# Optimization experiments

Measured on AMD Instinct MI355X. Metric: run time of the kernel, lower is better.

The kernel has to match this reference:

```python
import jax, jax.numpy as jnp
import numpy as np

K = 512      # fixed candidate budget per pyramid level (batched stand-in for mask.nonzero)
THR = 0.5    # candidate threshold from `p > 0.5`
CUBE = 4     # z-2 : z+2 -> 4-voxel cube per axis


def _conv3d(x, w, b, stride):
    y = jax.lax.conv_general_dilated(
        x, w, (stride, stride, stride), 'SAME',
        dimension_numbers=('NCDHW', 'OIDHW', 'NCDHW'))
    return y + b[None, :, None, None, None]


def _up2(x):
    return jnp.repeat(jnp.repeat(jnp.repeat(x, 2, axis=2), 2, axis=3), 2, axis=4)


def _extract(p):
    # p: [1, C, D, H, W] -> (cubes [K, C, 4, 4, 4], valid [K])
    p0 = p[0]
    C, D, H, W = p0.shape
    score = p0.max(axis=0)                       # [D, H, W] peak over channels
    vals, idx = jax.lax.top_k(score.reshape(-1), K)
    valid = (vals > THR).astype(p0.dtype)        # mask out sub-threshold slots
    z = idx // (H * W)
    rem = idx % (H * W)
    y = rem // W
    x = rem % W
    zs = jnp.clip(z - 2, 0, D - CUBE)
    ys = jnp.clip(y - 2, 0, H - CUBE)
    xs = jnp.clip(x - 2, 0, W - CUBE)

    def cube(zi, yi, xi):
        return jax.lax.dynamic_slice(p0, (0, zi, yi, xi), (C, CUBE, CUBE, CUBE))

    return jax.vmap(cube)(zs, ys, xs), valid


def _lhi(cubes):
    # local intensity descriptor: per-channel mean + std over the cube
    m = cubes.mean(axis=(2, 3, 4))
    s = jnp.sqrt(cubes.var(axis=(2, 3, 4)) + 1e-6)
    return jnp.concatenate([m, s], axis=-1)      # [K, 2C]


def _forward(x, c1w, c1b, c2w, c2b, c3w, c3b,
             l1w, l1b, l2w, l2b, l3w, l3b, w1, b1, w2, b2):
    # Encoder3D: 3 strided conv blocks
    f1 = jax.nn.relu(_conv3d(x, c1w, c1b, 2))    # [1,16,48,96,96]
    f2 = jax.nn.relu(_conv3d(f1, c2w, c2b, 2))   # [1,32,24,48,48]
    f3 = jax.nn.relu(_conv3d(f2, c3w, c3b, 2))   # [1,64,12,24,24]
    # FeaturePyramid3D: laterals + top-down adds
    p3 = _conv3d(f3, l3w, l3b, 1)
    p2 = _conv3d(f2, l2w, l2b, 1) + _up2(p3)
    p1 = _conv3d(f1, l1w, l1b, 1) + _up2(p2)
    outs = []
    for p in (p1, p2, p3):
        cubes, valid = _extract(p)
        lhi = _lhi(cubes)                        # [K, 64]
        h = jax.nn.relu(lhi @ w1 + b1)
        o = (h @ w2 + b2) * valid[:, None]       # zero out invalid candidate slots
        outs.append(o)
    return jnp.concatenate(outs, axis=0)         # [3K, 2]


def setup_inputs() -> dict:
    key = jax.random.key(0)
    ks = jax.random.split(key, 10)

    def w(k, shape, scale):
        return jax.random.normal(k, shape, jnp.float32) * scale

    return {
        'x':   jax.random.normal(ks[0], (1, 1, 96, 192, 192), jnp.float32),
        'c1w': w(ks[1], (16, 1, 3, 3, 3), 0.3),  'c1b': jnp.zeros((16,), jnp.float32),
        'c2w': w(ks[2], (32, 16, 3, 3, 3), 0.1), 'c2b': jnp.zeros((32,), jnp.float32),
        'c3w': w(ks[3], (64, 32, 3, 3, 3), 0.08), 'c3b': jnp.zeros((64,), jnp.float32),
        'l1w': w(ks[4], (32, 16, 1, 1, 1), 0.3), 'l1b': jnp.zeros((32,), jnp.float32),
        'l2w': w(ks[5], (32, 32, 1, 1, 1), 0.3), 'l2b': jnp.zeros((32,), jnp.float32),
        'l3w': w(ks[6], (32, 64, 1, 1, 1), 0.3), 'l3b': jnp.zeros((32,), jnp.float32),
        'w1':  w(ks[7], (64, 128), 0.2),         'b1':  jnp.zeros((128,), jnp.float32),
        'w2':  w(ks[8], (128, 2), 0.2),          'b2':  jnp.zeros((2,), jnp.float32),
    }


def reference(x, c1w, c1b, c2w, c2b, c3w, c3b,
              l1w, l1b, l2w, l2b, l3w, l3b, w1, b1, w2, b2):
    return _forward(x, c1w, c1b, c2w, c2b, c3w, c3b,
                    l1w, l1b, l2w, l2b, l3w, l3b, w1, b1, w2, b2)
```

## Files before the change

kernel.cpp:

```cpp
#include <hip/hip_runtime.h>
#include <hip/hip_bf16.h>
#include <cstdint>
#include <cstddef>

#define N1 442368
#define N2 55296
#define N3 6912

#define PZ1 9409
#define PN1 461041
#define PV1 461041
#define PZ2 2401
#define PN2 60025
#define PV2 60025

#define MAP1(x) (((x) & 1) ? 49 + ((x) >> 1) : ((x) >> 1))
#define MAP2(x) (((x) & 1) ? 25 + ((x) >> 1) : ((x) >> 1))

#define KCAND 512
#define CAP   4096

__device__ __forceinline__ unsigned long long f2key64(double f) {
  unsigned long long b = (unsigned long long)__double_as_longlong(f);
  return (b & 0x8000000000000000ULL) ? ~b : (b | 0x8000000000000000ULL);
}
__device__ __forceinline__ unsigned f2key32(float f) {
  unsigned b = __float_as_uint(f);
  return (b & 0x80000000u) ? ~b : (b | 0x80000000u);
}

__global__ void convert_k(const float* __restrict__ c1w, const float* __restrict__ c2w,
                          const float* __restrict__ c3w, const float* __restrict__ l1w,
                          const float* __restrict__ l2w, const float* __restrict__ l3w,
                          double* __restrict__ wd1, double* __restrict__ wd2,
                          double* __restrict__ wd3, double* __restrict__ wl1,
                          double* __restrict__ wl2, double* __restrict__ wl3) {
  int seg = blockIdx.y;
  int i = blockIdx.x * 256 + threadIdx.x;
  if (seg == 0) {
    if (i < 432) { int c = i & 15, t = i >> 4; wd1[i] = (double)c1w[c * 27 + t]; }
  } else if (seg == 1) {
    if (i < 13824) {
      int c = i & 31, t = (i >> 5) % 27, ci = i / 864;
      wd2[i] = (double)c2w[(c * 16 + ci) * 27 + t];
    }
  } else if (seg == 2) {
    if (i < 55296) {
      int c = i & 3, t = (i >> 2) % 27, ci = (i / 108) & 31, g = i / 3456;
      wd3[i] = (double)c3w[((g * 4 + c) * 32 + ci) * 27 + t];
    }
  } else if (seg == 3) {
    if (i < 512) { int c = i & 31, ci = i >> 5; wl1[i] = (double)l1w[c * 16 + ci]; }
  } else if (seg == 4) {
    if (i < 1024) { int c = i & 31, ci = i >> 5; wl2[i] = (double)l2w[c * 32 + ci]; }
  } else {
    if (i < 2048) { int c = i & 31, ci = i >> 5; wl3[i] = (double)l3w[c * 64 + ci]; }
  }
}

__global__ __launch_bounds__(256) void conv1_k(const float* __restrict__ x, const double* __restrict__ wd1,
                                               const float* __restrict__ b, double* __restrict__ f1) {
  int v = blockIdx.x * 256 + threadIdx.x;
  if (v >= PV1) return;
  int z = v / PZ1; int r = v % PZ1; int y = r / 97; int xo = r % 97;
  int ov = z * PZ1 + y * 97 + MAP1(xo);
  if (z >= 48 || y >= 96 || xo >= 96) {
#pragma unroll
    for (int c = 0; c < 16; c++) f1[(size_t)c * PN1 + ov] = 0.0;
    return;
  }
  float val[27];
#pragma unroll
  for (int dz = 0; dz < 3; dz++)
#pragma unroll
    for (int dy = 0; dy < 3; dy++)
#pragma unroll
      for (int dx = 0; dx < 3; dx++) {
        int zi = 2 * z + dz, yi = 2 * y + dy, xi = 2 * xo + dx;
        bool ok = (zi < 96) & (yi < 192) & (xi < 192);
        int zc = min(zi, 95), yc = min(yi, 191), xc = min(xi, 191);
        float t = x[(zc * 192 + yc) * 192 + xc];
        val[(dz * 3 + dy) * 3 + dx] = ok ? t : 0.0f;
      }
  double acc[16];
#pragma unroll
  for (int c = 0; c < 16; c++) acc[c] = (double)b[c];
#pragma unroll
  for (int t = 0; t < 27; t++) {
    double vv = (double)val[t];
#pragma unroll
    for (int c = 0; c < 16; c++) acc[c] = fma(vv, wd1[t * 16 + c], acc[c]);
  }
#pragma unroll
  for (int c = 0; c < 16; c++) f1[(size_t)c * PN1 + ov] = fmax(acc[c], 0.0);
}

__global__ __launch_bounds__(256, 2) void conv2_k(const double* __restrict__ f1, const double* __restrict__ wd2,
                                                  const float* __restrict__ b, double* __restrict__ f2) {
  int v = blockIdx.x * 256 + threadIdx.x;
  if (v >= PV2) return;
  int z = v / PZ2; int r = v % PZ2; int y = r / 49; int xo = r % 49;
  int ov = z * PZ2 + y * 49 + MAP2(xo);
  if (z >= 24 || y >= 48 || xo >= 48) {
#pragma unroll
    for (int c = 0; c < 32; c++) f2[(size_t)c * PN2 + ov] = 0.0;
    return;
  }
  double acc[32];
#pragma unroll
  for (int c = 0; c < 32; c++) acc[c] = (double)b[c];
  const double* base = f1 + (size_t)(2 * z) * PZ1 + (2 * y) * 97;
  for (int ci = 0; ci < 16; ci++) {
    const double* fp = base + (size_t)ci * PN1;
    double vals[27];
#pragma unroll
    for (int dz = 0; dz < 3; dz++)
#pragma unroll
      for (int dy = 0; dy < 3; dy++) {
        const double* row = fp + dz * PZ1 + dy * 97;
        int o = (dz * 3 + dy) * 3;
        vals[o + 0] = row[xo];
        vals[o + 1] = row[49 + xo];
        vals[o + 2] = row[xo + 1];
      }
#pragma unroll
    for (int t = 0; t < 27; t++) {
      double vv = vals[t];
      const double* w32 = wd2 + (ci * 27 + t) * 32;
#pragma unroll
      for (int c = 0; c < 32; c++) acc[c] = fma(vv, w32[c], acc[c]);
    }
  }
#pragma unroll
  for (int c = 0; c < 32; c++) f2[(size_t)c * PN2 + ov] = fmax(acc[c], 0.0);
}

__global__ __launch_bounds__(256, 2) void conv3_k(const double* __restrict__ f2, const double* __restrict__ wd3,
                                                  const float* __restrict__ b, double* __restrict__ f3) {
  int g = blockIdx.y;
  int v = blockIdx.x * 256 + threadIdx.x;
  if (v >= N3) return;
  int z = v / 576; int r = v % 576; int y = r / 24; int xo = r % 24;
  double acc[4];
#pragma unroll
  for (int c = 0; c < 4; c++) acc[c] = (double)b[g * 4 + c];
  const double* wp = wd3 + (size_t)g * 3456;
  const double* base = f2 + (size_t)(2 * z) * PZ2 + (2 * y) * 49;
  for (int ci = 0; ci < 32; ci++) {
    const double* fp = base + (size_t)ci * PN2;
    double vals[27];
#pragma unroll
    for (int dz = 0; dz < 3; dz++)
#pragma unroll
      for (int dy = 0; dy < 3; dy++) {
        const double* row = fp + dz * PZ2 + dy * 49;
        int o = (dz * 3 + dy) * 3;
        vals[o + 0] = row[xo];
        vals[o + 1] = row[25 + xo];
        vals[o + 2] = row[xo + 1];
      }
#pragma unroll
    for (int t = 0; t < 27; t++) {
      double vv = vals[t];
      const double* w4 = wp + (ci * 27 + t) * 4;
#pragma unroll
      for (int c = 0; c < 4; c++) acc[c] = fma(vv, w4[c], acc[c]);
    }
  }
#pragma unroll
  for (int c = 0; c < 4; c++) f3[(size_t)(g * 4 + c) * N3 + v] = fmax(acc[c], 0.0);
}

__global__ __launch_bounds__(256) void p3_k(const double* __restrict__ f3, const double* __restrict__ wl3,
                                            const float* __restrict__ b, double* __restrict__ p3d,
                                            float* __restrict__ p3f, double* __restrict__ s3,
                                            float* __restrict__ s3f) {
  int v = blockIdx.x * 256 + threadIdx.x;
  if (v >= N3) return;
  double acc[32];
#pragma unroll
  for (int c = 0; c < 32; c++) acc[c] = (double)b[c];
  for (int ci = 0; ci < 64; ci++) {
    double vv = f3[(size_t)ci * N3 + v];
    const double* wp = wl3 + ci * 32;
#pragma unroll
    for (int c = 0; c < 32; c++) acc[c] = fma(vv, wp[c], acc[c]);
  }
  double m = -1e300;
#pragma unroll
  for (int c = 0; c < 32; c++) {
    p3d[(size_t)c * N3 + v] = acc[c];
    p3f[(size_t)c * N3 + v] = (float)acc[c];
    m = fmax(m, acc[c]);
  }
  s3[v] = m;
  s3f[v] = (float)m;
}

__global__ __launch_bounds__(256) void p2_k(const double* __restrict__ f2, const double* __restrict__ wl2,
                                            const float* __restrict__ b, const double* __restrict__ p3d,
                                            double* __restrict__ p2d, float* __restrict__ p2f,
                                            double* __restrict__ s2, float* __restrict__ s2f) {
  int v = blockIdx.x * 256 + threadIdx.x;
  if (v >= N2) return;
  int z = v / (48 * 48); int r = v % (48 * 48); int y = r / 48; int xo = r % 48;
  int pidx = z * PZ2 + y * 49 + MAP2(xo);
  int up = ((z >> 1) * 24 + (y >> 1)) * 24 + (xo >> 1);
  double acc[32];
#pragma unroll
  for (int c = 0; c < 32; c++) acc[c] = (double)b[c];
  for (int ci = 0; ci < 32; ci++) {
    double vv = f2[(size_t)ci * PN2 + pidx];
    const double* wp = wl2 + ci * 32;
#pragma unroll
    for (int c = 0; c < 32; c++) acc[c] = fma(vv, wp[c], acc[c]);
  }
  double m = -1e300;
#pragma unroll
  for (int c = 0; c < 32; c++) {
    double o = acc[c] + p3d[(size_t)c * N3 + up];
    p2d[(size_t)c * N2 + v] = o;
    p2f[(size_t)c * N2 + v] = (float)o;
    m = fmax(m, o);
  }
  s2[v] = m;
  s2f[v] = (float)m;
}

__global__ __launch_bounds__(256) void p1_k(const double* __restrict__ f1, const double* __restrict__ wl1,
                                            const float* __restrict__ b, const double* __restrict__ p2d,
                                            double* __restrict__ s1, float* __restrict__ s1f) {
  int v = blockIdx.x * 256 + threadIdx.x;
  if (v >= N1) return;
  int z = v / (96 * 96); int r = v % (96 * 96); int y = r / 96; int xo = r % 96;
  int pidx = z * PZ1 + y * 97 + MAP1(xo);
  int up = ((z >> 1) * 48 + (y >> 1)) * 48 + (xo >> 1);
  double acc[32];
#pragma unroll
  for (int c = 0; c < 32; c++) acc[c] = (double)b[c];
  for (int ci = 0; ci < 16; ci++) {
    double vv = f1[(size_t)ci * PN1 + pidx];
    const double* wp = wl1 + ci * 32;
#pragma unroll
    for (int c = 0; c < 32; c++) acc[c] = fma(vv, wp[c], acc[c]);
  }
  double m = -1e300;
#pragma unroll
  for (int c = 0; c < 32; c++) m = fmax(m, acc[c] + p2d[(size_t)c * N2 + up]);
  s1[v] = m;
  s1f[v] = (float)m;
}

__global__ void hist1_k(const float* __restrict__ s1, const float* __restrict__ s2,
                        const float* __restrict__ s3, unsigned* __restrict__ hist) {
  int L = blockIdx.y;
  const float* s = L == 0 ? s1 : (L == 1 ? s2 : s3);
  int n = L == 0 ? N1 : (L == 1 ? N2 : N3);
  unsigned* hg = hist + L * 256;
  __shared__ unsigned h[256];
  h[threadIdx.x] = 0;
  __syncthreads();
  for (int i = blockIdx.x * 256 + threadIdx.x; i < n; i += gridDim.x * 256)
    atomicAdd(&h[f2key32(s[i]) >> 24], 1u);
  __syncthreads();
  unsigned v = h[threadIdx.x];
  if (v) atomicAdd(&hg[threadIdx.x], v);
}

__global__ void hist2_k(const float* __restrict__ s1, const float* __restrict__ s2,
                        const float* __restrict__ s3, const unsigned* __restrict__ hist1,
                        unsigned* __restrict__ hist2) {
  int L = blockIdx.y;
  const float* s = L == 0 ? s1 : (L == 1 ? s2 : s3);
  int n = L == 0 ? N1 : (L == 1 ? N2 : N3);
  const unsigned* h1 = hist1 + L * 256;
  unsigned run = 0; unsigned b1 = 0;
  for (int i = 255; i >= 0; i--) {
    unsigned c = h1[i];
    if (run + c >= (unsigned)KCAND) { b1 = (unsigned)i; break; }
    run += c;
  }
  unsigned* hg = hist2 + L * 256;
  __shared__ unsigned h[256];
  h[threadIdx.x] = 0;
  __syncthreads();
  for (int i = blockIdx.x * 256 + threadIdx.x; i < n; i += gridDim.x * 256) {
    unsigned k = f2key32(s[i]);
    if ((k >> 24) == b1) atomicAdd(&h[(k >> 16) & 255u], 1u);
  }
  __syncthreads();
  unsigned v = h[threadIdx.x];
  if (v) atomicAdd(&hg[threadIdx.x], v);
}

__global__ void compact_k(const float* __restrict__ s1f, const float* __restrict__ s2f,
                          const float* __restrict__ s3f,
                          const double* __restrict__ s1d, const double* __restrict__ s2d,
                          const double* __restrict__ s3d,
                          const unsigned* __restrict__ hist1, const unsigned* __restrict__ hist2,
                          unsigned long long* __restrict__ ck, unsigned* __restrict__ cidx,
                          unsigned* __restrict__ cnt) {
  int L = blockIdx.y;
  const float* s = L == 0 ? s1f : (L == 1 ? s2f : s3f);
  const double* sd = L == 0 ? s1d : (L == 1 ? s2d : s3d);
  int n = L == 0 ? N1 : (L == 1 ? N2 : N3);
  const unsigned* h1 = hist1 + L * 256;
  const unsigned* h2 = hist2 + L * 256;
  unsigned run = 0; unsigned b1 = 0;
  for (int i = 255; i >= 0; i--) {
    unsigned c = h1[i];
    if (run + c >= (unsigned)KCAND) { b1 = (unsigned)i; break; }
    run += c;
  }
  unsigned b2 = 0;
  for (int i = 255; i >= 0; i--) {
    run += h2[i];
    if (run >= (unsigned)KCAND) { b2 = (unsigned)i; break; }
  }
  unsigned T = (b1 << 24) | (b2 << 16);
  for (int i = blockIdx.x * 256 + threadIdx.x; i < n; i += gridDim.x * 256) {
    if (f2key32(s[i]) >= T) {
      unsigned pos = atomicAdd(&cnt[L], 1u);
      if (pos < (unsigned)CAP) {
        ck[(size_t)L * CAP + pos] = f2key64(sd[i]);
        cidx[(size_t)L * CAP + pos] = (unsigned)i;
      }
    }
  }
}

__global__ void sort_k(const unsigned long long* __restrict__ ckA, const unsigned* __restrict__ cidxA,
                       const unsigned* __restrict__ cnt, uint2* __restrict__ topkA) {
  __shared__ unsigned long long k_[CAP];
  __shared__ unsigned x_[CAP];
  int L = blockIdx.x;
  const unsigned long long* ck = ckA + (size_t)L * CAP;
  const unsigned* cidx = cidxA + (size_t)L * CAP;
  uint2* topk = topkA + (size_t)L * KCAND;
  int t = threadIdx.x;
  unsigned m = cnt[L]; if (m > (unsigned)CAP) m = CAP;
  int sz = 512; while (sz < (int)m) sz <<= 1;
  for (int i = t; i < sz; i += 1024) {
    if (i < (int)m) { k_[i] = ck[i]; x_[i] = cidx[i]; }
    else            { k_[i] = 0ULL;  x_[i] = 0xFFFFFFFFu; }
  }
  __syncthreads();
  for (int kk = 2; kk <= sz; kk <<= 1) {
    for (int j = kk >> 1; j > 0; j >>= 1) {
      for (int i = t; i < sz; i += 1024) {
        int l = i ^ j;
        if (l > i) {
          unsigned long long ka = k_[i], kb = k_[l];
          unsigned ia = x_[i], ib = x_[l];
          bool b_first = (kb > ka) || (kb == ka && ib < ia);
          bool up = (i & kk) == 0;
          if (up == b_first) { k_[i] = kb; x_[i] = ib; k_[l] = ka; x_[l] = ia; }
        }
      }
      __syncthreads();
    }
  }
  if (t < KCAND) {
    unsigned long long key = k_[t];
    unsigned long long bb = (key >> 63) ? (key & 0x7FFFFFFFFFFFFFFFULL) : ~key;
    double sc = __longlong_as_double((long long)bb);
    topk[t] = make_uint2(x_[t], sc > 0.5 ? 1u : 0u);
  }
}

__global__ __launch_bounds__(64) void mlp_k(const uint2* __restrict__ topkA,
                                            const double* __restrict__ f1d, const double* __restrict__ p2d,
                                            const float* __restrict__ p2f, const float* __restrict__ p3f,
                                            const double* __restrict__ wl1, const float* __restrict__ l1b,
                                            const float* __restrict__ w1, const float* __restrict__ b1,
                                            const float* __restrict__ w2, const float* __restrict__ b2,
                                            float* __restrict__ out) {
  __shared__ double lhi[64];
  __shared__ double f1c[16 * 64];
  __shared__ double wsD[16 * 32];
  int L = blockIdx.y;
  int s = blockIdx.x;
  int D = 48 >> L, H = 96 >> L, W = 96 >> L;
  uint2 e = topkA[(size_t)L * KCAND + s];
  unsigned idx = e.x;
  double valid = e.y ? 1.0 : 0.0;
  int HW = H * W;
  int z = (int)(idx / (unsigned)HW);
  int r = (int)(idx % (unsigned)HW);
  int y = r / W; int x = r % W;
  int zs = min(max(z - 2, 0), D - 4);
  int ys = min(max(y - 2, 0), H - 4);
  int xs = min(max(x - 2, 0), W - 4);
  int t = threadIdx.x;
  int c = t & 31, h = t >> 5;
  double sum = 0.0, ss = 0.0;
  if (L == 0) {
    for (int i = t; i < 512; i += 64) wsD[i] = wl1[i];
    for (int i = t; i < 1024; i += 64) {
      int ci = i >> 6, v = i & 63;
      int dz = v >> 4, dy = (v >> 2) & 3, dx = v & 3;
      f1c[i] = f1d[(size_t)ci * PN1 + (zs + dz) * PZ1 + (ys + dy) * 97 + MAP1(xs + dx)];
    }
    __syncthreads();
    double bc = (double)l1b[c];
    for (int i = 0; i < 32; i++) {
      int vv = h * 32 + i;
      int dz = vv >> 4, dy = (vv >> 2) & 3, dx = vv & 3;
      int up = (((zs + dz) >> 1) * 48 + ((ys + dy) >> 1)) * 48 + ((xs + dx) >> 1);
      double val = bc + p2d[(size_t)c * N2 + up];
#pragma unroll
      for (int ci = 0; ci < 16; ci++)
        val = fma(f1c[ci * 64 + vv], wsD[ci * 32 + c], val);
      sum += val; ss = fma(val, val, ss);
    }
  } else {
    const float* p = (L == 1) ? p2f : p3f;
    const float* pc = p + (size_t)c * D * HW;
    for (int i = 0; i < 32; i++) {
      int vv = h * 32 + i;
      int dz = vv >> 4, dy = (vv >> 2) & 3, dx = vv & 3;
      double val = (double)pc[(zs + dz) * HW + (ys + dy) * W + (xs + dx)];
      sum += val; ss = fma(val, val, ss);
    }
  }
  sum += __shfl_xor(sum, 32);
  ss  += __shfl_xor(ss, 32);
  if (h == 0) {
    double mean = sum * (1.0 / 64.0);
    double var = ss * (1.0 / 64.0) - mean * mean;
    lhi[c] = mean;
    lhi[32 + c] = sqrt(var + 1e-6);
  }
  __syncthreads();
  double h0 = (double)b1[t], h1 = (double)b1[t + 64];
  for (int i = 0; i < 64; i++) {
    double li = lhi[i];
    h0 = fma(li, (double)w1[i * 128 + t], h0);
    h1 = fma(li, (double)w1[i * 128 + t + 64], h1);
  }
  h0 = fmax(h0, 0.0); h1 = fmax(h1, 0.0);
  double o0 = h0 * (double)w2[t * 2 + 0] + h1 * (double)w2[(t + 64) * 2 + 0];
  double o1 = h0 * (double)w2[t * 2 + 1] + h1 * (double)w2[(t + 64) * 2 + 1];
  for (int o = 1; o < 64; o <<= 1) { o0 += __shfl_xor(o0, o); o1 += __shfl_xor(o1, o); }
  if (t == 0) {
    out[((size_t)L * KCAND + s) * 2 + 0] = (float)((o0 + (double)b2[0]) * valid);
    out[((size_t)L * KCAND + s) * 2 + 1] = (float)((o1 + (double)b2[1]) * valid);
  }
}

extern "C" void kernel_launch(void* const* d_in, const int* in_sizes, int n_in,
                              void* d_out, int out_size, void* d_ws, size_t ws_size,
                              hipStream_t stream) {
  const float* x   = (const float*)d_in[0];
  const float* c1w = (const float*)d_in[1];  const float* c1b = (const float*)d_in[2];
  const float* c2w = (const float*)d_in[3];  const float* c2b = (const float*)d_in[4];
  const float* c3w = (const float*)d_in[5];  const float* c3b = (const float*)d_in[6];
  const float* l1w = (const float*)d_in[7];  const float* l1b = (const float*)d_in[8];
  const float* l2w = (const float*)d_in[9];  const float* l2b = (const float*)d_in[10];
  const float* l3w = (const float*)d_in[11]; const float* l3b = (const float*)d_in[12];
  const float* w1  = (const float*)d_in[13]; const float* b1  = (const float*)d_in[14];
  const float* w2  = (const float*)d_in[15]; const float* b2  = (const float*)d_in[16];
  float* out = (float*)d_out;

  char* ws = (char*)d_ws;
  size_t off = 0;
  auto take = [&](size_t bytes) { size_t o = off; off = (off + bytes + 255) & ~(size_t)255; return o; };
  double* f1d = (double*)(ws + take((size_t)16 * PN1 * 8));
  double* f2d = (double*)(ws + take((size_t)32 * PN2 * 8));
  double* f3d = (double*)(ws + take((size_t)64 * N3 * 8));
  double* p2d = (double*)(ws + take((size_t)32 * N2 * 8));
  float*  p2f = (float*) (ws + take((size_t)32 * N2 * 4));
  double* p3d = (double*)(ws + take((size_t)32 * N3 * 8));
  float*  p3f = (float*) (ws + take((size_t)32 * N3 * 4));
  double* s1 = (double*)(ws + take((size_t)N1 * 8));
  double* s2 = (double*)(ws + take((size_t)N2 * 8));
  double* s3 = (double*)(ws + take((size_t)N3 * 8));
  float* s1f = (float*)(ws + take((size_t)N1 * 4));
  float* s2f = (float*)(ws + take((size_t)N2 * 4));
  float* s3f = (float*)(ws + take((size_t)N3 * 4));
  double* wd1 = (double*)(ws + take(432 * 8));
  double* wd2 = (double*)(ws + take(13824 * 8));
  double* wd3 = (double*)(ws + take(55296 * 8));
  double* wl1 = (double*)(ws + take(512 * 8));
  double* wl2 = (double*)(ws + take(1024 * 8));
  double* wl3 = (double*)(ws + take(2048 * 8));
  size_t zOff = take((3 * 256 + 3 * 256 + 3) * 4);
  unsigned* hist1 = (unsigned*)(ws + zOff);
  unsigned* hist2 = hist1 + 3 * 256;
  unsigned* cnt   = hist2 + 3 * 256;
  unsigned long long* candKey = (unsigned long long*)(ws + take((size_t)3 * CAP * 8));
  unsigned* candIdx = (unsigned*)(ws + take((size_t)3 * CAP * 4));
  uint2* topk = (uint2*)(ws + take((size_t)3 * KCAND * 8));

  hipMemsetAsync(ws + zOff, 0, (3 * 256 + 3 * 256 + 3) * 4, stream);

  convert_k<<<dim3(216, 6), 256, 0, stream>>>(c1w, c2w, c3w, l1w, l2w, l3w,
                                              wd1, wd2, wd3, wl1, wl2, wl3);
  conv1_k<<<(PV1 + 255) / 256, 256, 0, stream>>>(x, wd1, c1b, f1d);
  conv2_k<<<(PV2 + 255) / 256, 256, 0, stream>>>(f1d, wd2, c2b, f2d);
  conv3_k<<<dim3((N3 + 255) / 256, 16), 256, 0, stream>>>(f2d, wd3, c3b, f3d);
  p3_k<<<(N3 + 255) / 256, 256, 0, stream>>>(f3d, wl3, l3b, p3d, p3f, s3, s3f);
  p2_k<<<(N2 + 255) / 256, 256, 0, stream>>>(f2d, wl2, l2b, p3d, p2d, p2f, s2, s2f);
  p1_k<<<(N1 + 255) / 256, 256, 0, stream>>>(f1d, wl1, l1b, p2d, s1, s1f);

  hist1_k<<<dim3(64, 3), 256, 0, stream>>>(s1f, s2f, s3f, hist1);
  hist2_k<<<dim3(64, 3), 256, 0, stream>>>(s1f, s2f, s3f, hist1, hist2);
  compact_k<<<dim3(112, 3), 256, 0, stream>>>(s1f, s2f, s3f, s1, s2, s3, hist1, hist2,
                                              candKey, candIdx, cnt);
  sort_k<<<3, 1024, 0, stream>>>(candKey, candIdx, cnt, topk);
  mlp_k<<<dim3(KCAND, 3), 64, 0, stream>>>(topk, f1d, p2d, p2f, p3f, wl1, l1b,
                                           w1, b1, w2, b2, out);
}
```

Measured before the change: 429.6 us.

## Split conv2 across output-channel groups and batch loads ahead of FMAs with sched barriers

Conv2 now splits its 32 output channels into 4 groups of 8 on a second grid dimension. The weights are re-laid out per group, so each thread holds fewer accumulators and more blocks are launched. Across conv1/2/3 and the p1/p2/p3 lateral kernels, global loads are batched into register arrays and separated from the FMA chains by sched_barrier, and the channel loops are fully unrolled. The aim is more memory-level parallelism and higher occupancy. In exchange, conv2 re-reads its input patch once per channel group, and the unrolling raises register pressure.

```diff
diff --git a/kernel.cpp b/kernel.cpp
--- a/kernel.cpp
+++ b/kernel.cpp
@@ -19,6 +19,8 @@
 
 #define KCAND 512
 #define CAP   4096
+
+#define SBAR() __builtin_amdgcn_sched_barrier(0)
 
 __device__ __forceinline__ unsigned long long f2key64(double f) {
   unsigned long long b = (unsigned long long)__double_as_longlong(f);
@@ -41,8 +43,8 @@
     if (i < 432) { int c = i & 15, t = i >> 4; wd1[i] = (double)c1w[c * 27 + t]; }
   } else if (seg == 1) {
     if (i < 13824) {
-      int c = i & 31, t = (i >> 5) % 27, ci = i / 864;
-      wd2[i] = (double)c2w[(c * 16 + ci) * 27 + t];
+      int c = i & 7, t = (i >> 3) % 27, ci = (i / 216) & 15, g = i / 3456;
+      wd2[i] = (double)c2w[((g * 8 + c) * 16 + ci) * 27 + t];
     }
   } else if (seg == 2) {
     if (i < 55296) {
@@ -82,6 +84,7 @@
         float t = x[(zc * 192 + yc) * 192 + xc];
         val[(dz * 3 + dy) * 3 + dx] = ok ? t : 0.0f;
       }
+  SBAR();
   double acc[16];
 #pragma unroll
   for (int c = 0; c < 16; c++) acc[c] = (double)b[c];
@@ -95,21 +98,24 @@
   for (int c = 0; c < 16; c++) f1[(size_t)c * PN1 + ov] = fmax(acc[c], 0.0);
 }
 
-__global__ __launch_bounds__(256, 2) void conv2_k(const double* __restrict__ f1, const double* __restrict__ wd2,
-                                                  const float* __restrict__ b, double* __restrict__ f2) {
+__global__ __launch_bounds__(256) void conv2_k(const double* __restrict__ f1, const double* __restrict__ wd2,
+                                               const float* __restrict__ b, double* __restrict__ f2) {
+  int g = blockIdx.y;
   int v = blockIdx.x * 256 + threadIdx.x;
   if (v >= PV2) return;
   int z = v / PZ2; int r = v % PZ2; int y = r / 49; int xo = r % 49;
   int ov = z * PZ2 + y * 49 + MAP2(xo);
   if (z >= 24 || y >= 48 || xo >= 48) {
 #pragma unroll
-    for (int c = 0; c < 32; c++) f2[(size_t)c * PN2 + ov] = 0.0;
+    for (int c = 0; c < 8; c++) f2[(size_t)(g * 8 + c) * PN2 + ov] = 0.0;
     return;
   }
-  double acc[32];
-#pragma unroll
-  for (int c = 0; c < 32; c++) acc[c] = (double)b[c];
+  double acc[8];
+#pragma unroll
+  for (int c = 0; c < 8; c++) acc[c] = (double)b[g * 8 + c];
+  const double* wp = wd2 + (size_t)g * 3456;
   const double* base = f1 + (size_t)(2 * z) * PZ1 + (2 * y) * 97;
+#pragma unroll
   for (int ci = 0; ci < 16; ci++) {
     const double* fp = base + (size_t)ci * PN1;
     double vals[27];
@@ -123,20 +129,21 @@
         vals[o + 1] = row[49 + xo];
         vals[o + 2] = row[xo + 1];
       }
+    SBAR();
 #pragma unroll
     for (int t = 0; t < 27; t++) {
       double vv = vals[t];
-      const double* w32 = wd2 + (ci * 27 + t) * 32;
-#pragma unroll
-      for (int c = 0; c < 32; c++) acc[c] = fma(vv, w32[c], acc[c]);
-    }
-  }
-#pragma unroll
-  for (int c = 0; c < 32; c++) f2[(size_t)c * PN2 + ov] = fmax(acc[c], 0.0);
-}
-
-__global__ __launch_bounds__(256, 2) void conv3_k(const double* __restrict__ f2, const double* __restrict__ wd3,
-                                                  const float* __restrict__ b, double* __restrict__ f3) {
+      const double* w8 = wp + (ci * 27 + t) * 8;
+#pragma unroll
+      for (int c = 0; c < 8; c++) acc[c] = fma(vv, w8[c], acc[c]);
+    }
+  }
+#pragma unroll
+  for (int c = 0; c < 8; c++) f2[(size_t)(g * 8 + c) * PN2 + ov] = fmax(acc[c], 0.0);
+}
+
+__global__ __launch_bounds__(256) void conv3_k(const double* __restrict__ f2, const double* __restrict__ wd3,
+                                               const float* __restrict__ b, double* __restrict__ f3) {
   int g = blockIdx.y;
   int v = blockIdx.x * 256 + threadIdx.x;
   if (v >= N3) return;
@@ -146,6 +153,7 @@
   for (int c = 0; c < 4; c++) acc[c] = (double)b[g * 4 + c];
   const double* wp = wd3 + (size_t)g * 3456;
   const double* base = f2 + (size_t)(2 * z) * PZ2 + (2 * y) * 49;
+#pragma unroll
   for (int ci = 0; ci < 32; ci++) {
     const double* fp = base + (size_t)ci * PN2;
     double vals[27];
@@ -159,6 +167,7 @@
         vals[o + 1] = row[25 + xo];
         vals[o + 2] = row[xo + 1];
       }
+    SBAR();
 #pragma unroll
     for (int t = 0; t < 27; t++) {
       double vv = vals[t];
@@ -180,11 +189,18 @@
   double acc[32];
 #pragma unroll
   for (int c = 0; c < 32; c++) acc[c] = (double)b[c];
-  for (int ci = 0; ci < 64; ci++) {
-    double vv = f3[(size_t)ci * N3 + v];
-    const double* wp = wl3 + ci * 32;
-#pragma unroll
-    for (int c = 0; c < 32; c++) acc[c] = fma(vv, wp[c], acc[c]);
+#pragma unroll
+  for (int cb = 0; cb < 64; cb += 16) {
+    double vv[16];
+#pragma unroll
+    for (int j = 0; j < 16; j++) vv[j] = f3[(size_t)(cb + j) * N3 + v];
+    SBAR();
+#pragma unroll
+    for (int j = 0; j < 16; j++) {
+      const double* wpj = wl3 + (cb + j) * 32;
+#pragma unroll
+      for (int c = 0; c < 32; c++) acc[c] = fma(vv[j], wpj[c], acc[c]);
+    }
   }
   double m = -1e300;
 #pragma unroll
@@ -209,19 +225,33 @@
   double acc[32];
 #pragma unroll
   for (int c = 0; c < 32; c++) acc[c] = (double)b[c];
-  for (int ci = 0; ci < 32; ci++) {
-    double vv = f2[(size_t)ci * PN2 + pidx];
-    const double* wp = wl2 + ci * 32;
-#pragma unroll
-    for (int c = 0; c < 32; c++) acc[c] = fma(vv, wp[c], acc[c]);
+#pragma unroll
+  for (int cb = 0; cb < 32; cb += 16) {
+    double vv[16];
+#pragma unroll
+    for (int j = 0; j < 16; j++) vv[j] = f2[(size_t)(cb + j) * PN2 + pidx];
+    SBAR();
+#pragma unroll
+    for (int j = 0; j < 16; j++) {
+      const double* wpj = wl2 + (cb + j) * 32;
+#pragma unroll
+      for (int c = 0; c < 32; c++) acc[c] = fma(vv[j], wpj[c], acc[c]);
+    }
   }
   double m = -1e300;
 #pragma unroll
-  for (int c = 0; c < 32; c++) {
-    double o = acc[c] + p3d[(size_t)c * N3 + up];
-    p2d[(size_t)c * N2 + v] = o;
-    p2f[(size_t)c * N2 + v] = (float)o;
-    m = fmax(m, o);
+  for (int cb = 0; cb < 32; cb += 8) {
+    double pd[8];
+#pragma unroll
+    for (int j = 0; j < 8; j++) pd[j] = p3d[(size_t)(cb + j) * N3 + up];
+    SBAR();
+#pragma unroll
+    for (int j = 0; j < 8; j++) {
+      double o = acc[cb + j] + pd[j];
+      p2d[(size_t)(cb + j) * N2 + v] = o;
+      p2f[(size_t)(cb + j) * N2 + v] = (float)o;
+      m = fmax(m, o);
+    }
   }
   s2[v] = m;
   s2f[v] = (float)m;
@@ -235,18 +265,29 @@
   int z = v / (96 * 96); int r = v % (96 * 96); int y = r / 96; int xo = r % 96;
   int pidx = z * PZ1 + y * 97 + MAP1(xo);
   int up = ((z >> 1) * 48 + (y >> 1)) * 48 + (xo >> 1);
+  double vv[16];
+#pragma unroll
+  for (int j = 0; j < 16; j++) vv[j] = f1[(size_t)j * PN1 + pidx];
+  SBAR();
   double acc[32];
 #pragma unroll
   for (int c = 0; c < 32; c++) acc[c] = (double)b[c];
-  for (int ci = 0; ci < 16; ci++) {
-    double vv = f1[(size_t)ci * PN1 + pidx];
-    const double* wp = wl1 + ci * 32;
-#pragma unroll
-    for (int c = 0; c < 32; c++) acc[c] = fma(vv, wp[c], acc[c]);
+#pragma unroll
+  for (int j = 0; j < 16; j++) {
+    const double* wpj = wl1 + j * 32;
+#pragma unroll
+    for (int c = 0; c < 32; c++) acc[c] = fma(vv[j], wpj[c], acc[c]);
   }
   double m = -1e300;
 #pragma unroll
-  for (int c = 0; c < 32; c++) m = fmax(m, acc[c] + p2d[(size_t)c * N2 + up]);
+  for (int cb = 0; cb < 32; cb += 8) {
+    double pd[8];
+#pragma unroll
+    for (int j = 0; j < 8; j++) pd[j] = p2d[(size_t)(cb + j) * N2 + up];
+    SBAR();
+#pragma unroll
+    for (int j = 0; j < 8; j++) m = fmax(m, acc[cb + j] + pd[j]);
+  }
   s1[v] = m;
   s1f[v] = (float)m;
 }
@@ -497,7 +538,7 @@
   convert_k<<<dim3(216, 6), 256, 0, stream>>>(c1w, c2w, c3w, l1w, l2w, l3w,
                                               wd1, wd2, wd3, wl1, wl2, wl3);
   conv1_k<<<(PV1 + 255) / 256, 256, 0, stream>>>(x, wd1, c1b, f1d);
-  conv2_k<<<(PV2 + 255) / 256, 256, 0, stream>>>(f1d, wd2, c2b, f2d);
+  conv2_k<<<dim3((PV2 + 255) / 256, 4), 256, 0, stream>>>(f1d, wd2, c2b, f2d);
   conv3_k<<<dim3((N3 + 255) / 256, 16), 256, 0, stream>>>(f2d, wd3, c3b, f3d);
   p3_k<<<(N3 + 255) / 256, 256, 0, stream>>>(f3d, wl3, l3b, p3d, p3f, s3, s3f);
   p2_k<<<(N2 + 255) / 256, 256, 0, stream>>>(f2d, wl2, l2b, p3d, p2d, p2f, s2, s2f);
```

Result: no change. 433.0 us (+0.8%).

## Tile conv2 through double-buffered LDS rows and split conv3 input channels

Applied to the files above, without the earlier changes.

conv2 now runs one block per output (z,y) row. The block stages the 9 input rows of each input channel into double-buffered shared memory, and each wave computes 8 output channels, so the f1 reads are reused across channels. conv3 splits its 32 input channels into two halves that write separate partial buffers, which doubles the grid; p3 then sums the halves and applies ReLU. The histogram memset is folded into the weight-convert kernel, which removes one API call but adds an extra buffer and extra reads in p3.

```diff
diff --git a/kernel.cpp b/kernel.cpp
--- a/kernel.cpp
+++ b/kernel.cpp
@@ -34,27 +34,31 @@
                           const float* __restrict__ l2w, const float* __restrict__ l3w,
                           double* __restrict__ wd1, double* __restrict__ wd2,
                           double* __restrict__ wd3, double* __restrict__ wl1,
-                          double* __restrict__ wl2, double* __restrict__ wl3) {
+                          double* __restrict__ wl2, double* __restrict__ wl3,
+                          unsigned* __restrict__ zero_base) {
   int seg = blockIdx.y;
   int i = blockIdx.x * 256 + threadIdx.x;
   if (seg == 0) {
     if (i < 432) { int c = i & 15, t = i >> 4; wd1[i] = (double)c1w[c * 27 + t]; }
   } else if (seg == 1) {
     if (i < 13824) {
-      int c = i & 31, t = (i >> 5) % 27, ci = i / 864;
-      wd2[i] = (double)c2w[(c * 16 + ci) * 27 + t];
+      int c = i & 7, t = (i >> 3) % 27, ci = (i / 216) & 15, g = i / 3456;
+      wd2[i] = (double)c2w[((g * 8 + c) * 16 + ci) * 27 + t];
     }
   } else if (seg == 2) {
     if (i < 55296) {
-      int c = i & 3, t = (i >> 2) % 27, ci = (i / 108) & 31, g = i / 3456;
-      wd3[i] = (double)c3w[((g * 4 + c) * 32 + ci) * 27 + t];
+      int c = i & 3, t = (i >> 2) % 27, ci = (i / 108) & 15, gi = i / 1728;
+      int g = gi & 15, cig = gi >> 4;
+      wd3[i] = (double)c3w[((g * 4 + c) * 32 + cig * 16 + ci) * 27 + t];
     }
   } else if (seg == 3) {
     if (i < 512) { int c = i & 31, ci = i >> 5; wl1[i] = (double)l1w[c * 16 + ci]; }
   } else if (seg == 4) {
     if (i < 1024) { int c = i & 31, ci = i >> 5; wl2[i] = (double)l2w[c * 32 + ci]; }
+  } else if (seg == 5) {
+    if (i < 2048) { int c = i & 31, ci = i >> 5; wl3[i] = (double)l3w[c * 64 + ci]; }
   } else {
-    if (i < 2048) { int c = i & 31, ci = i >> 5; wl3[i] = (double)l3w[c * 64 + ci]; }
+    if (i < 3 * 256 + 3 * 256 + 3) zero_base[i] = 0u;
   }
 }
 
@@ -95,58 +99,89 @@
   for (int c = 0; c < 16; c++) f1[(size_t)c * PN1 + ov] = fmax(acc[c], 0.0);
 }
 
-__global__ __launch_bounds__(256, 2) void conv2_k(const double* __restrict__ f1, const double* __restrict__ wd2,
-                                                  const float* __restrict__ b, double* __restrict__ f2) {
-  int v = blockIdx.x * 256 + threadIdx.x;
-  if (v >= PV2) return;
-  int z = v / PZ2; int r = v % PZ2; int y = r / 49; int xo = r % 49;
-  int ov = z * PZ2 + y * 49 + MAP2(xo);
-  if (z >= 24 || y >= 48 || xo >= 48) {
-#pragma unroll
-    for (int c = 0; c < 32; c++) f2[(size_t)c * PN2 + ov] = 0.0;
+__global__ __launch_bounds__(256) void conv2_k(const double* __restrict__ f1, const double* __restrict__ wd2,
+                                               const float* __restrict__ b, double* __restrict__ f2) {
+  __shared__ double st[2][9 * 97];
+  int z = blockIdx.x;
+  int y = blockIdx.y;
+  int tid = threadIdx.x;
+  if (z >= 24 || y >= 48) {
+    for (int i = tid; i < 32 * 49; i += 256) {
+      int c = i / 49, s = i % 49;
+      f2[(size_t)c * PN2 + z * PZ2 + y * 49 + s] = 0.0;
+    }
     return;
   }
-  double acc[32];
-#pragma unroll
-  for (int c = 0; c < 32; c++) acc[c] = (double)b[c];
+  int wave = __builtin_amdgcn_readfirstlane(tid >> 6);
+  int lane = tid & 63;
+  int e0 = tid, e1 = tid + 256, e2 = tid + 512, e3 = tid + 768;
+  auto goff = [](int e) {
+    int r = e / 97, c = e % 97;
+    return (size_t)(r / 3) * PZ1 + (size_t)(r % 3) * 97 + (size_t)c;
+  };
+  size_t g0 = goff(e0), g1 = goff(e1), g2 = goff(e2), g3 = goff(e3 < 873 ? e3 : 0);
   const double* base = f1 + (size_t)(2 * z) * PZ1 + (2 * y) * 97;
+  st[0][e0] = base[g0];
+  st[0][e1] = base[g1];
+  st[0][e2] = base[g2];
+  if (e3 < 873) st[0][e3] = base[g3];
+  double acc[8];
+  const double* wp = wd2 + (size_t)wave * 3456;
+#pragma unroll
+  for (int c = 0; c < 8; c++) acc[c] = (double)b[wave * 8 + c];
+  int xo = min(lane, 48);
   for (int ci = 0; ci < 16; ci++) {
-    const double* fp = base + (size_t)ci * PN1;
-    double vals[27];
+    __syncthreads();
+    int cur = ci & 1;
+    if (ci + 1 < 16) {
+      const double* nb = base + (size_t)(ci + 1) * PN1;
+      int nxt = cur ^ 1;
+      st[nxt][e0] = nb[g0];
+      st[nxt][e1] = nb[g1];
+      st[nxt][e2] = nb[g2];
+      if (e3 < 873) st[nxt][e3] = nb[g3];
+    }
 #pragma unroll
     for (int dz = 0; dz < 3; dz++)
 #pragma unroll
       for (int dy = 0; dy < 3; dy++) {
-        const double* row = fp + dz * PZ1 + dy * 97;
-        int o = (dz * 3 + dy) * 3;
-        vals[o + 0] = row[xo];
-        vals[o + 1] = row[49 + xo];
-        vals[o + 2] = row[xo + 1];
+        const double* row = &st[cur][(dz * 3 + dy) * 97];
+        double t0 = row[xo], t1 = row[49 + xo], t2 = row[xo + 1];
+        int tb = (dz * 3 + dy) * 3;
+        const double* w0 = wp + (ci * 27 + tb) * 8;
+        const double* w1 = wp + (ci * 27 + tb + 1) * 8;
+        const double* w2 = wp + (ci * 27 + tb + 2) * 8;
+#pragma unroll
+        for (int c = 0; c < 8; c++) acc[c] = fma(t0, w0[c], acc[c]);
+#pragma unroll
+        for (int c = 0; c < 8; c++) acc[c] = fma(t1, w1[c], acc[c]);
+#pragma unroll
+        for (int c = 0; c < 8; c++) acc[c] = fma(t2, w2[c], acc[c]);
       }
-#pragma unroll
-    for (int t = 0; t < 27; t++) {
-      double vv = vals[t];
-      const double* w32 = wd2 + (ci * 27 + t) * 32;
-#pragma unroll
-      for (int c = 0; c < 32; c++) acc[c] = fma(vv, w32[c], acc[c]);
-    }
-  }
-#pragma unroll
-  for (int c = 0; c < 32; c++) f2[(size_t)c * PN2 + ov] = fmax(acc[c], 0.0);
-}
-
-__global__ __launch_bounds__(256, 2) void conv3_k(const double* __restrict__ f2, const double* __restrict__ wd3,
-                                                  const float* __restrict__ b, double* __restrict__ f3) {
-  int g = blockIdx.y;
+  }
+  if (lane < 49) {
+    int ov = z * PZ2 + y * 49 + MAP2(xo);
+    bool real = lane < 48;
+#pragma unroll
+    for (int c = 0; c < 8; c++)
+      f2[(size_t)(wave * 8 + c) * PN2 + ov] = real ? fmax(acc[c], 0.0) : 0.0;
+  }
+}
+
+__global__ __launch_bounds__(256) void conv3_k(const double* __restrict__ f2, const double* __restrict__ wd3,
+                                               const float* __restrict__ b, double* __restrict__ f3a,
+                                               double* __restrict__ f3b) {
+  int gi = blockIdx.y;
+  int g = gi & 15, cig = gi >> 4;
   int v = blockIdx.x * 256 + threadIdx.x;
   if (v >= N3) return;
   int z = v / 576; int r = v % 576; int y = r / 24; int xo = r % 24;
   double acc[4];
 #pragma unroll
-  for (int c = 0; c < 4; c++) acc[c] = (double)b[g * 4 + c];
-  const double* wp = wd3 + (size_t)g * 3456;
-  const double* base = f2 + (size_t)(2 * z) * PZ2 + (2 * y) * 49;
-  for (int ci = 0; ci < 32; ci++) {
+  for (int c = 0; c < 4; c++) acc[c] = cig == 0 ? (double)b[g * 4 + c] : 0.0;
+  const double* wp = wd3 + (size_t)gi * 1728;
+  const double* base = f2 + (size_t)(cig * 16) * PN2 + (size_t)(2 * z) * PZ2 + (2 * y) * 49;
+  for (int ci = 0; ci < 16; ci++) {
     const double* fp = base + (size_t)ci * PN2;
     double vals[27];
 #pragma unroll
@@ -167,11 +202,13 @@
       for (int c = 0; c < 4; c++) acc[c] = fma(vv, w4[c], acc[c]);
     }
   }
-#pragma unroll
-  for (int c = 0; c < 4; c++) f3[(size_t)(g * 4 + c) * N3 + v] = fmax(acc[c], 0.0);
-}
-
-__global__ __launch_bounds__(256) void p3_k(const double* __restrict__ f3, const double* __restrict__ wl3,
+  double* dst = cig == 0 ? f3a : f3b;
+#pragma unroll
+  for (int c = 0; c < 4; c++) dst[(size_t)(g * 4 + c) * N3 + v] = acc[c];
+}
+
+__global__ __launch_bounds__(256) void p3_k(const double* __restrict__ f3a, const double* __restrict__ f3b,
+                                            const double* __restrict__ wl3,
                                             const float* __restrict__ b, double* __restrict__ p3d,
                                             float* __restrict__ p3f, double* __restrict__ s3,
                                             float* __restrict__ s3f) {
@@ -181,7 +218,7 @@
 #pragma unroll
   for (int c = 0; c < 32; c++) acc[c] = (double)b[c];
   for (int ci = 0; ci < 64; ci++) {
-    double vv = f3[(size_t)ci * N3 + v];
+    double vv = fmax(f3a[(size_t)ci * N3 + v] + f3b[(size_t)ci * N3 + v], 0.0);
     const double* wp = wl3 + ci * 32;
 #pragma unroll
     for (int c = 0; c < 32; c++) acc[c] = fma(vv, wp[c], acc[c]);
@@ -467,7 +504,8 @@
   auto take = [&](size_t bytes) { size_t o = off; off = (off + bytes + 255) & ~(size_t)255; return o; };
   double* f1d = (double*)(ws + take((size_t)16 * PN1 * 8));
   double* f2d = (double*)(ws + take((size_t)32 * PN2 * 8));
-  double* f3d = (double*)(ws + take((size_t)64 * N3 * 8));
+  double* f3a = (double*)(ws + take((size_t)64 * N3 * 8));
+  double* f3b = (double*)(ws + take((size_t)64 * N3 * 8));
   double* p2d = (double*)(ws + take((size_t)32 * N2 * 8));
   float*  p2f = (float*) (ws + take((size_t)32 * N2 * 4));
   double* p3d = (double*)(ws + take((size_t)32 * N3 * 8));
@@ -492,14 +530,12 @@
   unsigned* candIdx = (unsigned*)(ws + take((size_t)3 * CAP * 4));
   uint2* topk = (uint2*)(ws + take((size_t)3 * KCAND * 8));
 
-  hipMemsetAsync(ws + zOff, 0, (3 * 256 + 3 * 256 + 3) * 4, stream);
-
-  convert_k<<<dim3(216, 6), 256, 0, stream>>>(c1w, c2w, c3w, l1w, l2w, l3w,
-                                              wd1, wd2, wd3, wl1, wl2, wl3);
+  convert_k<<<dim3(216, 7), 256, 0, stream>>>(c1w, c2w, c3w, l1w, l2w, l3w,
+                                              wd1, wd2, wd3, wl1, wl2, wl3, hist1);
   conv1_k<<<(PV1 + 255) / 256, 256, 0, stream>>>(x, wd1, c1b, f1d);
-  conv2_k<<<(PV2 + 255) / 256, 256, 0, stream>>>(f1d, wd2, c2b, f2d);
-  conv3_k<<<dim3((N3 + 255) / 256, 16), 256, 0, stream>>>(f2d, wd3, c3b, f3d);
-  p3_k<<<(N3 + 255) / 256, 256, 0, stream>>>(f3d, wl3, l3b, p3d, p3f, s3, s3f);
+  conv2_k<<<dim3(25, 49), 256, 0, stream>>>(f1d, wd2, c2b, f2d);
+  conv3_k<<<dim3((N3 + 255) / 256, 32), 256, 0, stream>>>(f2d, wd3, c3b, f3a, f3b);
+  p3_k<<<(N3 + 255) / 256, 256, 0, stream>>>(f3a, f3b, wl3, l3b, p3d, p3f, s3, s3f);
   p2_k<<<(N2 + 255) / 256, 256, 0, stream>>>(f2d, wl2, l2b, p3d, p2d, p2f, s2, s2f);
   p1_k<<<(N1 + 255) / 256, 256, 0, stream>>>(f1d, wl1, l1b, p2d, s1, s1f);
 
```

Measured after the change: 388.3 us. 9.6% less time.
